# Optimization experiments

Hardware: AMD Instinct MI355X
Metric: run time of the kernel (lower is better)

## Reference

```python
import jax, jax.numpy as jnp
import numpy as np

D_MODEL = 1024
NUM_HEADS = 16
D_HEAD = D_MODEL // NUM_HEADS
SCALE = D_HEAD ** -0.5
B, S = 2, 2048


def setup_inputs() -> dict:
    key = jax.random.key(0)
    ks = jax.random.split(key, 9)
    # Xavier-uniform-like scale for square weights: sqrt(6/(fan_in+fan_out))
    lim = float(np.sqrt(6.0 / (D_MODEL + D_MODEL)))
    def w(k):
        return jax.random.uniform(k, (D_MODEL, D_MODEL), jnp.float32, -lim, lim)
    def b(k):
        return jax.random.normal(k, (D_MODEL,), jnp.float32) * 0.02
    return {
        "query": jax.random.normal(ks[0], (B, S, D_MODEL), jnp.float32),
        "Wq": w(ks[1]), "bq": b(ks[2]),
        "Wk": w(ks[3]), "bk": b(ks[4]),
        "Wv": w(ks[5]), "bv": b(ks[6]),
        "Wo": w(ks[7]), "bo": b(ks[8]),
    }


def reference(query, Wq, bq, Wk, bk, Wv, bv, Wo, bo):
    Bsz, Sl, _ = query.shape
    # torch Linear: y = x @ W.T + b
    q = query @ Wq.T + bq
    k = query @ Wk.T + bk
    v = query @ Wv.T + bv
    # split heads -> [B, H, S, Dh]
    def split(t):
        return t.reshape(Bsz, Sl, NUM_HEADS, D_HEAD).transpose(0, 2, 1, 3)
    q, k, v = split(q), split(k), split(v)
    # regular attention path: full [B,H,S,S] score matrix, no causal mask
    attn_weights = jnp.einsum("bhqd,bhkd->bhqk", q, k) * SCALE
    attn_probs = jax.nn.softmax(attn_weights, axis=-1)
    attn_output = jnp.einsum("bhqk,bhkd->bhqd", attn_probs, v)
    # merge heads
    merged = attn_output.transpose(0, 2, 1, 3).reshape(Bsz, Sl, D_MODEL)
    return merged @ Wo.T + bo
```

## Files before the change

kernel.cpp:

```cpp
#include <hip/hip_runtime.h>
#include <cstdint>
#include <cstddef>

typedef __bf16 bf16;
typedef __bf16 bf16x8 __attribute__((ext_vector_type(8)));
typedef float f32x4 __attribute__((ext_vector_type(4)));

#define DMODEL 1024
#define HEADS  16
#define DH     64
#define BATCH  2
#define SEQ    2048
#define MTOT   (BATCH*SEQ)
#define LDQKV  3072

typedef __attribute__((address_space(1))) void gas_void;
typedef __attribute__((address_space(3))) void las_void;
#define GLOAD_LDS(gsrc, ldst) \
  __builtin_amdgcn_global_load_lds((gas_void*)(gsrc), (las_void*)(ldst), 16, 0, 0)

__device__ __forceinline__ f32x4 mfma16(bf16x8 a, bf16x8 b, f32x4 c) {
  return __builtin_amdgcn_mfma_f32_16x16x32_bf16(a, b, c, 0, 0, 0);
}

__device__ __forceinline__ bf16x8 cvt8(float4 a, float4 b) {
  bf16x8 v;
  v[0] = (bf16)a.x; v[1] = (bf16)a.y; v[2] = (bf16)a.z; v[3] = (bf16)a.w;
  v[4] = (bf16)b.x; v[5] = (bf16)b.y; v[6] = (bf16)b.z; v[7] = (bf16)b.w;
  return v;
}

__global__ __launch_bounds__(256) void k_prep(
    const float* __restrict__ x, const float* __restrict__ Wq, const float* __restrict__ Wk,
    const float* __restrict__ Wv, const float* __restrict__ bq, const float* __restrict__ bk,
    const float* __restrict__ bv, const float* __restrict__ Wo,
    bf16* __restrict__ xbf, bf16* __restrict__ Wqkv, float* __restrict__ bqkv,
    bf16* __restrict__ wo) {
  const int blk = blockIdx.x, tid = threadIdx.x;
  if (blk < 2048) {
    const int i = blk * 256 + tid;
    const float4* p = (const float4*)x;
    ((bf16x8*)xbf)[i] = cvt8(p[2*i], p[2*i+1]);
  } else if (blk < 3584) {
    const int i = (blk - 2048) * 256 + tid;
    const int row = i >> 7;
    const int c   = (i & 127) * 8;
    const float* src;
    if (row < 1024)       src = Wq + (size_t)row * 1024 + c;
    else if (row < 2048)  src = Wk + (size_t)(row - 1024) * 1024 + c;
    else                  src = Wv + (size_t)(row - 2048) * 1024 + c;
    float4 a = ((const float4*)src)[0], b = ((const float4*)src)[1];
    ((bf16x8*)Wqkv)[i] = cvt8(a, b);
    if (i < 3072) {
      float bb;
      if (i < 1024)      bb = bq[i];
      else if (i < 2048) bb = bk[i - 1024];
      else               bb = bv[i - 2048];
      bqkv[i] = bb;
    }
  } else {
    const int i = (blk - 3584) * 256 + tid;
    const float4* p = (const float4*)Wo;
    ((bf16x8*)wo)[i] = cvt8(p[2*i], p[2*i+1]);
  }
}

template <int QSCALE, int OUTF32>
__global__ __launch_bounds__(256) void k_gemm_bt(const bf16* __restrict__ A,
                                                 const bf16* __restrict__ B,
                                                 const float* __restrict__ bias,
                                                 void* __restrict__ Cout,
                                                 int N, int K) {
  __shared__ bf16 Alds[128 * 32];
  __shared__ bf16 Blds[128 * 32];
  const int tid  = threadIdx.x;
  const int lane = tid & 63;
  const int w    = tid >> 6;
  const int wr   = w >> 1, wc = w & 1;
  const int l15  = lane & 15, lg = lane >> 4;
  const int bm = blockIdx.x, bn = blockIdx.y;

  f32x4 acc[4][4];
#pragma unroll
  for (int i = 0; i < 4; ++i)
#pragma unroll
    for (int j = 0; j < 4; ++j) acc[i][j] = (f32x4){0.f, 0.f, 0.f, 0.f};

  const int r = tid >> 2;
  const int c = (tid & 3) * 8;
  const bf16* aptr0 = A + ((size_t)bm * 128 + r) * K + c;
  const bf16* aptr1 = A + ((size_t)bm * 128 + 64 + r) * K + c;
  const bf16* bptr0 = B + ((size_t)bn * 128 + r) * K + c;
  const bf16* bptr1 = B + ((size_t)bn * 128 + 64 + r) * K + c;

  for (int kt = 0; kt < K / 32; ++kt) {
    __syncthreads();
    GLOAD_LDS(aptr0, Alds + tid * 8);
    GLOAD_LDS(aptr1, Alds + 2048 + tid * 8);
    GLOAD_LDS(bptr0, Blds + tid * 8);
    GLOAD_LDS(bptr1, Blds + 2048 + tid * 8);
    aptr0 += 32; aptr1 += 32; bptr0 += 32; bptr1 += 32;
    __syncthreads();

    bf16x8 af[4], bfr[4];
#pragma unroll
    for (int i = 0; i < 4; ++i)
      af[i] = *(const bf16x8*)(Alds + (wr * 64 + i * 16 + l15) * 32 + lg * 8);
#pragma unroll
    for (int j = 0; j < 4; ++j)
      bfr[j] = *(const bf16x8*)(Blds + (wc * 64 + j * 16 + l15) * 32 + lg * 8);
#pragma unroll
    for (int i = 0; i < 4; ++i)
#pragma unroll
      for (int j = 0; j < 4; ++j)
        acc[i][j] = mfma16(af[i], bfr[j], acc[i][j]);
  }

#pragma unroll
  for (int j = 0; j < 4; ++j) {
    const int col = bn * 128 + wc * 64 + j * 16 + l15;
    const float bv = bias[col];
    const float scale = (QSCALE && col < 1024) ? 0.125f : 1.0f;
#pragma unroll
    for (int i = 0; i < 4; ++i) {
      const int row0 = bm * 128 + wr * 64 + i * 16 + lg * 4;
#pragma unroll
      for (int rr = 0; rr < 4; ++rr) {
        const float v = (acc[i][j][rr] + bv) * scale;
        const size_t off = (size_t)(row0 + rr) * N + col;
        if (OUTF32) ((float*)Cout)[off] = v;
        else        ((bf16*)Cout)[off]  = (bf16)v;
      }
    }
  }
}

__global__ __launch_bounds__(256) void k_transpose_v(const bf16* __restrict__ qkv,
                                                     bf16* __restrict__ vt) {
  __shared__ bf16 tile[64][72];
  const int bh = blockIdx.x, st = blockIdx.y;
  const int b = bh >> 4, h = bh & 15;
  const int tid = threadIdx.x;
  const int r = tid >> 2, c0 = (tid & 3) * 16;
  const bf16* src = qkv + (size_t)(b * SEQ + st * 64 + r) * LDQKV + 2048 + h * DH + c0;
  *(bf16x8*)&tile[r][c0]     = ((const bf16x8*)src)[0];
  *(bf16x8*)&tile[r][c0 + 8] = ((const bf16x8*)src)[1];
  __syncthreads();
  const int d = tid >> 2, s0 = (tid & 3) * 16;
  bf16x8 o0, o1;
#pragma unroll
  for (int j = 0; j < 8; ++j) o0[j] = tile[s0 + j][d];
#pragma unroll
  for (int j = 0; j < 8; ++j) o1[j] = tile[s0 + 8 + j][d];
  bf16* dst = vt + ((size_t)bh * DH + d) * SEQ + st * 64 + s0;
  *(bf16x8*)dst       = o0;
  *(bf16x8*)(dst + 8) = o1;
}

__global__ __launch_bounds__(256) void k_attn(const bf16* __restrict__ qkv,
                                              const bf16* __restrict__ vt,
                                              bf16* __restrict__ attnout) {
  __shared__ bf16 Klds[2][64 * 64];
  __shared__ bf16 Vtlds[2][64 * 64];
  __shared__ bf16 Plds[4][32 * 64];

  const int orig = blockIdx.x;
  const int wgid = (orig & 7) * 64 + (orig >> 3);
  const int bh = wgid >> 4;
  const int qt = wgid & 15;
  const int b = bh >> 4, h = bh & 15;
  const int tid = threadIdx.x;
  const int lane = tid & 63, w = tid >> 6;
  const int l15 = lane & 15, lg = lane >> 4;
  const int r7 = l15 & 7;
  const int qbase = qt * 128 + w * 32;

  const int sr = tid >> 3;
  const int ss = tid & 7;

  auto STAGE = [&](int buf, int t) {
    const int kb = t * 64;
#pragma unroll
    for (int u = 0; u < 2; ++u) {
      const int row = u * 32 + sr;
      const int slot = ss ^ (row & 7);
      const bf16* ksrc = qkv + (size_t)(b * SEQ + kb + row) * LDQKV + 1024 + h * DH + slot * 8;
      GLOAD_LDS(ksrc, Klds[buf] + u * 2048 + tid * 8);
      const bf16* vsrc = vt + ((size_t)bh * DH + row) * SEQ + kb + slot * 8;
      GLOAD_LDS(vsrc, Vtlds[buf] + u * 2048 + tid * 8);
    }
  };

  bf16x8 qf[2][2];
#pragma unroll
  for (int i = 0; i < 2; ++i)
#pragma unroll
    for (int kc = 0; kc < 2; ++kc)
      qf[i][kc] = *(const bf16x8*)(qkv + (size_t)(b * SEQ + qbase + i * 16 + l15) * LDQKV
                                   + h * DH + kc * 32 + lg * 8);

  f32x4 oacc[2][4];
#pragma unroll
  for (int i = 0; i < 2; ++i)
#pragma unroll
    for (int dt = 0; dt < 4; ++dt) oacc[i][dt] = (f32x4){0.f, 0.f, 0.f, 0.f};

  float m_r[2][4], l_r[2][4];
#pragma unroll
  for (int i = 0; i < 2; ++i)
#pragma unroll
    for (int rr = 0; rr < 4; ++rr) { m_r[i][rr] = -1e30f; l_r[i][rr] = 0.f; }

  STAGE(0, 0);
  __syncthreads();

  int cur = 0;
  for (int t = 0; t < SEQ / 64; ++t) {
    if (t + 1 < SEQ / 64) STAGE(cur ^ 1, t + 1);

    const bf16* Kb  = Klds[cur];
    const bf16* Vb  = Vtlds[cur];

    f32x4 sacc[2][4];
    __builtin_amdgcn_s_setprio(1);
#pragma unroll
    for (int kt = 0; kt < 4; ++kt) {
      const bf16* krow = Kb + (kt * 16 + l15) * 64;
      bf16x8 kf0 = *(const bf16x8*)(krow + ((lg ^ r7) * 8));
      bf16x8 kf1 = *(const bf16x8*)(krow + (((4 + lg) ^ r7) * 8));
#pragma unroll
      for (int i = 0; i < 2; ++i) {
        f32x4 z = (f32x4){0.f, 0.f, 0.f, 0.f};
        z = mfma16(qf[i][0], kf0, z);
        z = mfma16(qf[i][1], kf1, z);
        sacc[i][kt] = z;
      }
    }
    __builtin_amdgcn_s_setprio(0);

    float p[2][4][4];
#pragma unroll
    for (int i = 0; i < 2; ++i) {
#pragma unroll
      for (int rr = 0; rr < 4; ++rr) {
        float mx = fmaxf(fmaxf(sacc[i][0][rr], sacc[i][1][rr]),
                         fmaxf(sacc[i][2][rr], sacc[i][3][rr]));
        mx = fmaxf(mx, __shfl_xor(mx, 1));
        mx = fmaxf(mx, __shfl_xor(mx, 2));
        mx = fmaxf(mx, __shfl_xor(mx, 4));
        mx = fmaxf(mx, __shfl_xor(mx, 8));
        const float mnew = fmaxf(m_r[i][rr], mx);
        const float alpha = __expf(m_r[i][rr] - mnew);
        float rs = 0.f;
#pragma unroll
        for (int kt = 0; kt < 4; ++kt) {
          const float e = __expf(sacc[i][kt][rr] - mnew);
          p[i][kt][rr] = e;
          rs += e;
        }
        rs += __shfl_xor(rs, 1);
        rs += __shfl_xor(rs, 2);
        rs += __shfl_xor(rs, 4);
        rs += __shfl_xor(rs, 8);
        l_r[i][rr] = l_r[i][rr] * alpha + rs;
        m_r[i][rr] = mnew;
#pragma unroll
        for (int dt = 0; dt < 4; ++dt)
          oacc[i][dt][rr] = oacc[i][dt][rr] * alpha;
      }
    }

    char* pb = (char*)Plds[w];
#pragma unroll
    for (int i = 0; i < 2; ++i)
#pragma unroll
      for (int kt = 0; kt < 4; ++kt)
#pragma unroll
        for (int rr = 0; rr < 4; ++rr) {
          const int q = i * 16 + lg * 4 + rr;
          const int k = kt * 16 + l15;
          const int off = (q * 128 + k * 2) ^ ((q & 7) << 4);
          *(bf16*)(pb + off) = (bf16)p[i][kt][rr];
        }

    bf16x8 pa[2][2];
#pragma unroll
    for (int i = 0; i < 2; ++i) {
      const bf16* prow = (const bf16*)Plds[w] + (i * 16 + l15) * 64;
      pa[i][0] = *(const bf16x8*)(prow + ((lg ^ r7) * 8));
      pa[i][1] = *(const bf16x8*)(prow + (((4 + lg) ^ r7) * 8));
    }
    __builtin_amdgcn_s_setprio(1);
#pragma unroll
    for (int dt = 0; dt < 4; ++dt) {
      const bf16* vrow = Vb + (dt * 16 + l15) * 64;
      bf16x8 vf0 = *(const bf16x8*)(vrow + ((lg ^ r7) * 8));
      bf16x8 vf1 = *(const bf16x8*)(vrow + (((4 + lg) ^ r7) * 8));
#pragma unroll
      for (int i = 0; i < 2; ++i) {
        oacc[i][dt] = mfma16(pa[i][0], vf0, oacc[i][dt]);
        oacc[i][dt] = mfma16(pa[i][1], vf1, oacc[i][dt]);
      }
    }
    __builtin_amdgcn_s_setprio(0);

    __syncthreads();
    cur ^= 1;
  }

#pragma unroll
  for (int i = 0; i < 2; ++i)
#pragma unroll
    for (int rr = 0; rr < 4; ++rr) {
      const float inv = 1.0f / l_r[i][rr];
      const int row = qbase + i * 16 + lg * 4 + rr;
#pragma unroll
      for (int dt = 0; dt < 4; ++dt)
        attnout[(size_t)(b * SEQ + row) * DMODEL + h * DH + dt * 16 + l15] =
            (bf16)(oacc[i][dt][rr] * inv);
    }
}

extern "C" void kernel_launch(void* const* d_in, const int* in_sizes, int n_in,
                              void* d_out, int out_size, void* d_ws, size_t ws_size,
                              hipStream_t stream) {
  (void)in_sizes; (void)n_in; (void)out_size; (void)ws_size;
  const float* query = (const float*)d_in[0];
  const float* Wq = (const float*)d_in[1];
  const float* bq = (const float*)d_in[2];
  const float* Wk = (const float*)d_in[3];
  const float* bk = (const float*)d_in[4];
  const float* Wv = (const float*)d_in[5];
  const float* bv = (const float*)d_in[6];
  const float* Wo = (const float*)d_in[7];
  const float* bo = (const float*)d_in[8];

  char* ws = (char*)d_ws;
  bf16*  xbf  = (bf16*)(ws);
  bf16*  attn = (bf16*)(ws);
  bf16*  wqkv = (bf16*)(ws + 8388608);
  bf16*  wo   = (bf16*)(ws + 14680064);
  float* bqkv = (float*)(ws + 16777216);
  bf16*  qkv  = (bf16*)(ws + 16842752);
  bf16*  vt   = (bf16*)(ws + 42008576);

  k_prep<<<4096, 256, 0, stream>>>(query, Wq, Wk, Wv, bq, bk, bv, Wo,
                                   xbf, wqkv, bqkv, wo);
  k_gemm_bt<1, 0><<<dim3(32, 24), 256, 0, stream>>>(xbf, wqkv, bqkv, (void*)qkv, 3072, 1024);
  k_transpose_v<<<dim3(32, 32), 256, 0, stream>>>(qkv, vt);
  k_attn<<<512, 256, 0, stream>>>(qkv, vt, attn);
  k_gemm_bt<0, 1><<<dim3(32, 8), 256, 0, stream>>>(attn, wo, bo, d_out, 1024, 1024);
}
```

Baseline: 263.7 us.

## Halve attention query tile, add lazy max rescaling and deferred row-sum reduction

The attention kernel now gives each wave 16 query rows instead of 32 and doubles the grid to 1024 workgroups, so K/V tiles are reused across fewer queries but occupancy and parallelism go up. Online softmax rescaling of the accumulator is skipped unless some row's max grows by more than 8 (a conditional, wave-uniform branch). The per-tile shuffle reduction of the row sum is replaced by per-lane partial sums that are reduced once at the end. The cost is twice the K/V LDS staging traffic in total, plus looser numerical bounds on exp values.

```diff
diff --git a/kernel.cpp b/kernel.cpp
--- a/kernel.cpp
+++ b/kernel.cpp
@@ -162,18 +162,18 @@
                                               bf16* __restrict__ attnout) {
   __shared__ bf16 Klds[2][64 * 64];
   __shared__ bf16 Vtlds[2][64 * 64];
-  __shared__ bf16 Plds[4][32 * 64];
+  __shared__ bf16 Plds[4][16 * 64];
 
   const int orig = blockIdx.x;
-  const int wgid = (orig & 7) * 64 + (orig >> 3);
-  const int bh = wgid >> 4;
-  const int qt = wgid & 15;
+  const int wgid = (orig & 7) * 128 + (orig >> 3);
+  const int bh = wgid >> 5;
+  const int qt = wgid & 31;
   const int b = bh >> 4, h = bh & 15;
   const int tid = threadIdx.x;
   const int lane = tid & 63, w = tid >> 6;
   const int l15 = lane & 15, lg = lane >> 4;
   const int r7 = l15 & 7;
-  const int qbase = qt * 128 + w * 32;
+  const int qbase = qt * 64 + w * 16;
 
   const int sr = tid >> 3;
   const int ss = tid & 7;
@@ -191,25 +191,18 @@
     }
   };
 
-  bf16x8 qf[2][2];
-#pragma unroll
-  for (int i = 0; i < 2; ++i)
-#pragma unroll
-    for (int kc = 0; kc < 2; ++kc)
-      qf[i][kc] = *(const bf16x8*)(qkv + (size_t)(b * SEQ + qbase + i * 16 + l15) * LDQKV
-                                   + h * DH + kc * 32 + lg * 8);
-
-  f32x4 oacc[2][4];
-#pragma unroll
-  for (int i = 0; i < 2; ++i)
-#pragma unroll
-    for (int dt = 0; dt < 4; ++dt) oacc[i][dt] = (f32x4){0.f, 0.f, 0.f, 0.f};
-
-  float m_r[2][4], l_r[2][4];
-#pragma unroll
-  for (int i = 0; i < 2; ++i)
-#pragma unroll
-    for (int rr = 0; rr < 4; ++rr) { m_r[i][rr] = -1e30f; l_r[i][rr] = 0.f; }
+  bf16x8 qf[2];
+#pragma unroll
+  for (int kc = 0; kc < 2; ++kc)
+    qf[kc] = *(const bf16x8*)(qkv + (size_t)(b * SEQ + qbase + l15) * LDQKV
+                              + h * DH + kc * 32 + lg * 8);
+
+  f32x4 oacc[4];
+#pragma unroll
+  for (int dt = 0; dt < 4; ++dt) oacc[dt] = (f32x4){0.f, 0.f, 0.f, 0.f};
+  float m_r[4], l_r[4];
+#pragma unroll
+  for (int rr = 0; rr < 4; ++rr) { m_r[rr] = -1e30f; l_r[rr] = 0.f; }
 
   STAGE(0, 0);
   __syncthreads();
@@ -218,89 +211,79 @@
   for (int t = 0; t < SEQ / 64; ++t) {
     if (t + 1 < SEQ / 64) STAGE(cur ^ 1, t + 1);
 
-    const bf16* Kb  = Klds[cur];
-    const bf16* Vb  = Vtlds[cur];
-
-    f32x4 sacc[2][4];
+    const bf16* Kb = Klds[cur];
+    const bf16* Vb = Vtlds[cur];
+
+    f32x4 sacc[4];
     __builtin_amdgcn_s_setprio(1);
 #pragma unroll
     for (int kt = 0; kt < 4; ++kt) {
       const bf16* krow = Kb + (kt * 16 + l15) * 64;
       bf16x8 kf0 = *(const bf16x8*)(krow + ((lg ^ r7) * 8));
       bf16x8 kf1 = *(const bf16x8*)(krow + (((4 + lg) ^ r7) * 8));
-#pragma unroll
-      for (int i = 0; i < 2; ++i) {
-        f32x4 z = (f32x4){0.f, 0.f, 0.f, 0.f};
-        z = mfma16(qf[i][0], kf0, z);
-        z = mfma16(qf[i][1], kf1, z);
-        sacc[i][kt] = z;
+      f32x4 z = (f32x4){0.f, 0.f, 0.f, 0.f};
+      z = mfma16(qf[0], kf0, z);
+      z = mfma16(qf[1], kf1, z);
+      sacc[kt] = z;
+    }
+    __builtin_amdgcn_s_setprio(0);
+
+    float mx[4];
+    int need = 0;
+#pragma unroll
+    for (int rr = 0; rr < 4; ++rr) {
+      float m3 = fmaxf(fmaxf(sacc[0][rr], sacc[1][rr]),
+                       fmaxf(sacc[2][rr], sacc[3][rr]));
+      m3 = fmaxf(m3, __shfl_xor(m3, 1));
+      m3 = fmaxf(m3, __shfl_xor(m3, 2));
+      m3 = fmaxf(m3, __shfl_xor(m3, 4));
+      m3 = fmaxf(m3, __shfl_xor(m3, 8));
+      mx[rr] = m3;
+      need |= (m3 > m_r[rr] + 8.0f);
+    }
+    if (__any(need)) {
+#pragma unroll
+      for (int rr = 0; rr < 4; ++rr) {
+        const float mnew = fmaxf(m_r[rr], mx[rr]);
+        const float alpha = __expf(m_r[rr] - mnew);
+        l_r[rr] *= alpha;
+#pragma unroll
+        for (int dt = 0; dt < 4; ++dt) oacc[dt][rr] *= alpha;
+        m_r[rr] = mnew;
       }
     }
-    __builtin_amdgcn_s_setprio(0);
-
-    float p[2][4][4];
-#pragma unroll
-    for (int i = 0; i < 2; ++i) {
+    float p[4][4];
+#pragma unroll
+    for (int rr = 0; rr < 4; ++rr)
+#pragma unroll
+      for (int kt = 0; kt < 4; ++kt) {
+        const float e = __expf(sacc[kt][rr] - m_r[rr]);
+        p[kt][rr] = e;
+        l_r[rr] += e;
+      }
+
+    char* pb = (char*)Plds[w];
+#pragma unroll
+    for (int kt = 0; kt < 4; ++kt)
 #pragma unroll
       for (int rr = 0; rr < 4; ++rr) {
-        float mx = fmaxf(fmaxf(sacc[i][0][rr], sacc[i][1][rr]),
-                         fmaxf(sacc[i][2][rr], sacc[i][3][rr]));
-        mx = fmaxf(mx, __shfl_xor(mx, 1));
-        mx = fmaxf(mx, __shfl_xor(mx, 2));
-        mx = fmaxf(mx, __shfl_xor(mx, 4));
-        mx = fmaxf(mx, __shfl_xor(mx, 8));
-        const float mnew = fmaxf(m_r[i][rr], mx);
-        const float alpha = __expf(m_r[i][rr] - mnew);
-        float rs = 0.f;
-#pragma unroll
-        for (int kt = 0; kt < 4; ++kt) {
-          const float e = __expf(sacc[i][kt][rr] - mnew);
-          p[i][kt][rr] = e;
-          rs += e;
-        }
-        rs += __shfl_xor(rs, 1);
-        rs += __shfl_xor(rs, 2);
-        rs += __shfl_xor(rs, 4);
-        rs += __shfl_xor(rs, 8);
-        l_r[i][rr] = l_r[i][rr] * alpha + rs;
-        m_r[i][rr] = mnew;
-#pragma unroll
-        for (int dt = 0; dt < 4; ++dt)
-          oacc[i][dt][rr] = oacc[i][dt][rr] * alpha;
+        const int q = lg * 4 + rr;
+        const int k = kt * 16 + l15;
+        const int off = (q * 128 + k * 2) ^ ((q & 7) << 4);
+        *(bf16*)(pb + off) = (bf16)p[kt][rr];
       }
-    }
-
-    char* pb = (char*)Plds[w];
-#pragma unroll
-    for (int i = 0; i < 2; ++i)
-#pragma unroll
-      for (int kt = 0; kt < 4; ++kt)
-#pragma unroll
-        for (int rr = 0; rr < 4; ++rr) {
-          const int q = i * 16 + lg * 4 + rr;
-          const int k = kt * 16 + l15;
-          const int off = (q * 128 + k * 2) ^ ((q & 7) << 4);
-          *(bf16*)(pb + off) = (bf16)p[i][kt][rr];
-        }
-
-    bf16x8 pa[2][2];
-#pragma unroll
-    for (int i = 0; i < 2; ++i) {
-      const bf16* prow = (const bf16*)Plds[w] + (i * 16 + l15) * 64;
-      pa[i][0] = *(const bf16x8*)(prow + ((lg ^ r7) * 8));
-      pa[i][1] = *(const bf16x8*)(prow + (((4 + lg) ^ r7) * 8));
-    }
+
+    const bf16* prow = (const bf16*)Plds[w] + l15 * 64;
+    bf16x8 pa0 = *(const bf16x8*)(prow + ((lg ^ r7) * 8));
+    bf16x8 pa1 = *(const bf16x8*)(prow + (((4 + lg) ^ r7) * 8));
     __builtin_amdgcn_s_setprio(1);
 #pragma unroll
     for (int dt = 0; dt < 4; ++dt) {
       const bf16* vrow = Vb + (dt * 16 + l15) * 64;
       bf16x8 vf0 = *(const bf16x8*)(vrow + ((lg ^ r7) * 8));
       bf16x8 vf1 = *(const bf16x8*)(vrow + (((4 + lg) ^ r7) * 8));
-#pragma unroll
-      for (int i = 0; i < 2; ++i) {
-        oacc[i][dt] = mfma16(pa[i][0], vf0, oacc[i][dt]);
-        oacc[i][dt] = mfma16(pa[i][1], vf1, oacc[i][dt]);
-      }
+      oacc[dt] = mfma16(pa0, vf0, oacc[dt]);
+      oacc[dt] = mfma16(pa1, vf1, oacc[dt]);
     }
     __builtin_amdgcn_s_setprio(0);
 
@@ -309,16 +292,19 @@
   }
 
 #pragma unroll
-  for (int i = 0; i < 2; ++i)
-#pragma unroll
-    for (int rr = 0; rr < 4; ++rr) {
-      const float inv = 1.0f / l_r[i][rr];
-      const int row = qbase + i * 16 + lg * 4 + rr;
-#pragma unroll
-      for (int dt = 0; dt < 4; ++dt)
-        attnout[(size_t)(b * SEQ + row) * DMODEL + h * DH + dt * 16 + l15] =
-            (bf16)(oacc[i][dt][rr] * inv);
-    }
+  for (int rr = 0; rr < 4; ++rr) {
+    float rs = l_r[rr];
+    rs += __shfl_xor(rs, 1);
+    rs += __shfl_xor(rs, 2);
+    rs += __shfl_xor(rs, 4);
+    rs += __shfl_xor(rs, 8);
+    const float inv = 1.0f / rs;
+    const int row = qbase + lg * 4 + rr;
+#pragma unroll
+    for (int dt = 0; dt < 4; ++dt)
+      attnout[(size_t)(b * SEQ + row) * DMODEL + h * DH + dt * 16 + l15] =
+          (bf16)(oacc[dt][rr] * inv);
+  }
 }
 
 extern "C" void kernel_launch(void* const* d_in, const int* in_sizes, int n_in,
@@ -348,6 +334,6 @@
                                    xbf, wqkv, bqkv, wo);
   k_gemm_bt<1, 0><<<dim3(32, 24), 256, 0, stream>>>(xbf, wqkv, bqkv, (void*)qkv, 3072, 1024);
   k_transpose_v<<<dim3(32, 32), 256, 0, stream>>>(qkv, vt);
-  k_attn<<<512, 256, 0, stream>>>(qkv, vt, attn);
+  k_attn<<<1024, 256, 0, stream>>>(qkv, vt, attn);
   k_gemm_bt<0, 1><<<dim3(32, 8), 256, 0, stream>>>(attn, wo, bo, d_out, 1024, 1024);
 }
```

New measurement: 239.5 us. 9.1% less time.
